# Performance work log

Hardware: AMD Instinct MI355X
Metric: run time of the kernel (lower is better)

The kernel has to match this reference:

```python
import jax, jax.numpy as jnp
import numpy as np

VOCAB = 128

def setup_inputs() -> dict:
    key = jax.random.key(0)
    k1, k2, k3, k4 = jax.random.split(key, 4)
    B, S, H = 64, 512, 1024
    x = jax.random.randint(k1, (B, S), 0, VOCAB, dtype=jnp.int32)
    h = jnp.zeros((B, H), dtype=jnp.float32)
    # Xavier-normal-ish scaled params
    W_xh = jax.random.normal(k2, (VOCAB, H), dtype=jnp.float32) * (2.0 / (VOCAB + H)) ** 0.5
    W_hh = jax.random.normal(k3, (H, H), dtype=jnp.float32) * (1.0 / H) ** 0.5
    b_h = jnp.zeros((H,), dtype=jnp.float32)
    W_out = jax.random.normal(k4, (H, VOCAB), dtype=jnp.float32) * (1.0 / H) ** 0.5
    b_out = jnp.zeros((VOCAB,), dtype=jnp.float32)
    return {"x": x, "h": h, "W_xh": W_xh, "W_hh": W_hh, "b_h": b_h,
            "W_out": W_out, "b_out": b_out}

def reference(x, h, W_xh, W_hh, b_h, W_out, b_out):
    """x: (B,S) int32, h: (B,H). Returns (logits (B,S,V), h_final (B,H)).
    one_hot(x) @ W_xh == embedding gather W_xh[x] (same math, no dense one-hot).
    Dropout is identity (eval mode). Sequential tanh recurrence via lax.scan."""
    x_emb = W_xh[x]                      # (B, S, H) gather == one-hot matmul
    x_emb_t = jnp.swapaxes(x_emb, 0, 1)  # (S, B, H) scan over time

    def step(h, xe):
        h_new = jnp.tanh(xe + h @ W_hh + b_h)
        return h_new, h_new

    h_final, hidden = jax.lax.scan(step, h, x_emb_t)  # hidden: (S, B, H)
    hidden = jnp.swapaxes(hidden, 0, 1)               # (B, S, H)
    logits = hidden @ W_out + b_out                   # (B, S, V)
    return logits, h_final
```

## Files before the change

kernel.cpp:

```cpp
#include <hip/hip_runtime.h>
#include <hip/hip_bf16.h>
#include <stdint.h>


#define Bz 64
#define Sz 512
#define Hz 1024
#define Vz 128
#define NWG 64
#define COLS 32
#define WGT 512

typedef __attribute__((ext_vector_type(8)))  short short8;
typedef __attribute__((ext_vector_type(16))) float f32x16;
typedef __attribute__((ext_vector_type(4)))  unsigned u32x4;

__device__ __align__(16) unsigned short g_hfrag[3][2][64][64][8];
__device__ __align__(16) unsigned short g_hidden[(size_t)Sz*2*64*64*8];
__device__ __align__(16) unsigned short g_wout[64*4*64*8];

__device__ __forceinline__ unsigned short f2bf(float f) {
  union { float f; unsigned u; } v; v.f = f;
  unsigned r = v.u + 0x7FFFu + ((v.u >> 16) & 1u);
  return (unsigned short)(r >> 16);
}

__device__ __forceinline__ float fast_tanh(float x) {
  float cx = fminf(9.0f, fmaxf(-9.0f, x));
  float e  = __builtin_amdgcn_exp2f(cx * 2.88539008178f);
  return (e - 1.0f) * __builtin_amdgcn_rcpf(e + 1.0f);
}

__device__ __forceinline__ void load8_nodrain(const unsigned short* p0, u32x4 t[8]) {
  const unsigned short* p1 = p0 + 2048;
  asm volatile(
    "global_load_dwordx4 %0, %8, off sc1\n\t"
    "global_load_dwordx4 %1, %8, off offset:1024 sc1\n\t"
    "global_load_dwordx4 %2, %8, off offset:2048 sc1\n\t"
    "global_load_dwordx4 %3, %8, off offset:3072 sc1\n\t"
    "global_load_dwordx4 %4, %9, off sc1\n\t"
    "global_load_dwordx4 %5, %9, off offset:1024 sc1\n\t"
    "global_load_dwordx4 %6, %9, off offset:2048 sc1\n\t"
    "global_load_dwordx4 %7, %9, off offset:3072 sc1"
    : "=&v"(t[0]), "=&v"(t[1]), "=&v"(t[2]), "=&v"(t[3]),
      "=&v"(t[4]), "=&v"(t[5]), "=&v"(t[6]), "=&v"(t[7])
    : "v"(p0), "v"(p1)
    : "memory");
}

__device__ __forceinline__ void store16_sc1(unsigned short* p, u32x4 v) {
  asm volatile("global_store_dwordx4 %0, %1, off sc1" :: "v"(p), "v"(v) : "memory");
}
__device__ __forceinline__ void store4_sc1(unsigned short* p, unsigned v) {
  asm volatile("global_store_dword %0, %1, off sc1" :: "v"(p), "v"(v) : "memory");
}

__global__ void pack_wout(const float* __restrict__ W_out) {
  int gid = blockIdx.x * blockDim.x + threadIdx.x;
  int lane = gid & 63;
  int nt   = (gid >> 6) & 3;
  int kb   = gid >> 8;
  int n = nt * 32 + (lane & 31);
  int k0 = kb * 16 + (lane >> 5) * 8;
  unsigned short t[8];
#pragma unroll
  for (int j = 0; j < 8; ++j)
    t[j] = f2bf(W_out[(size_t)(k0 + j) * Vz + n]);
  uint4 w;
  w.x = (unsigned)t[0] | ((unsigned)t[1] << 16);
  w.y = (unsigned)t[2] | ((unsigned)t[3] << 16);
  w.z = (unsigned)t[4] | ((unsigned)t[5] << 16);
  w.w = (unsigned)t[6] | ((unsigned)t[7] << 16);
  *(uint4*)&g_wout[(size_t)gid * 8] = w;
}

__global__ __launch_bounds__(WGT) void rnn_persistent(
    const int* __restrict__ x, const float* __restrict__ h0,
    const float* __restrict__ W_xh, const float* __restrict__ W_hh,
    const float* __restrict__ b_h, float* __restrict__ out,
    unsigned* __restrict__ flags)
{
  __shared__ unsigned short ldsW[64 * 64 * 8];
  __shared__ float red[8 * 1024];

  const int g    = blockIdx.x;
  const int bh   = g >> 5;
  const int cg   = g & 31;
  const int n0g  = cg * COLS;
  const int tid  = threadIdx.x;
  const int lane = tid & 63;
  const int ki   = tid >> 6;
  const int bn   = lane & 31;

  for (int idx = tid; idx < 64 * 64; idx += WGT) {
    int kb = idx >> 6, L = idx & 63;
    int n = L & 31, kq = L >> 5;
    unsigned short t[8];
#pragma unroll
    for (int j = 0; j < 8; ++j)
      t[j] = f2bf(W_hh[(size_t)(kb * 16 + kq * 8 + j) * Hz + n0g + n]);
    uint4 w;
    w.x = (unsigned)t[0] | ((unsigned)t[1] << 16);
    w.y = (unsigned)t[2] | ((unsigned)t[3] << 16);
    w.z = (unsigned)t[4] | ((unsigned)t[5] << 16);
    w.w = (unsigned)t[6] | ((unsigned)t[7] << 16);
    *(uint4*)&ldsW[(size_t)idx * 8] = w;
  }

  if (tid < 128) {
    int s_idx = g * 128 + tid;
    int fbh = s_idx >> 12, fkb = (s_idx >> 6) & 63, fL = s_idx & 63;
    int m = fbh * 32 + (fL & 31);
    int k = fkb * 16 + (fL >> 5) * 8;
    const float* src = &h0[(size_t)m * Hz + k];
    float4 a0 = *(const float4*)&src[0];
    float4 a1 = *(const float4*)&src[4];
    u32x4 w;
    w.x = (unsigned)f2bf(a0.x) | ((unsigned)f2bf(a0.y) << 16);
    w.y = (unsigned)f2bf(a0.z) | ((unsigned)f2bf(a0.w) << 16);
    w.z = (unsigned)f2bf(a1.x) | ((unsigned)f2bf(a1.y) << 16);
    w.w = (unsigned)f2bf(a1.z) | ((unsigned)f2bf(a1.w) << 16);
    store16_sc1(&g_hfrag[0][fbh][fkb][fL][0], w);
  }

  __syncthreads();
  asm volatile("s_waitcnt vmcnt(0)" ::: "memory");
  if (lane == 0)
    __hip_atomic_store(&flags[(g * 8 + ki) * 4], 1u, __ATOMIC_RELAXED,
                       __HIP_MEMORY_SCOPE_AGENT);

  const int er   = tid & 31;
  const int em   = bh * 32 + er;
  const int c0   = (tid >> 5) * 2;
  const int kcol = n0g + c0;
  const int kb_g = kcol >> 4;
  const int kq2  = (kcol >> 3) & 1;
  const int lslot = kq2 * 32 + er;
  const size_t slotOff =
      (((size_t)bh * 64 + kb_g) * 64 + lslot) * 8 + (kcol & 7);
  const float bias0 = b_h[kcol], bias1 = b_h[kcol + 1];

  const int pflag =
      ((bh * 32 + ki * 4 + (lane >> 3)) * 8 + (lane & 7)) * 4;

  int tok_n = x[em * Sz];
  float2 xv_n = *(const float2*)&W_xh[(size_t)tok_n * Hz + kcol];

  int rp = 0;
  for (int s = 0; s < Sz; ++s) {
    const int wp = (rp == 2) ? 0 : rp + 1;
    const unsigned tgt = (unsigned)(s + 1);

    {
      for (int it = 0; it < 65536; ++it) {
        unsigned v = 0xFFFFFFFFu;
        if (lane < 32)
          v = __hip_atomic_load(&flags[pflag], __ATOMIC_RELAXED,
                                __HIP_MEMORY_SCOPE_AGENT);
        if (__all(v >= tgt)) break;
        __builtin_amdgcn_s_sleep(1);
      }
      asm volatile("" ::: "memory");
    }

    u32x4 t[8];
    load8_nodrain(&g_hfrag[rp][bh][ki * 8][lane][0], t);
    f32x16 acc0 = {}, acc1 = {};

#define STAGE(J, CNT)                                                          \
    {                                                                          \
      asm volatile("s_waitcnt vmcnt(" #CNT ")"                                 \
                   : "+v"(t[2 * (J)]), "+v"(t[2 * (J) + 1]));                  \
      const int kbp = ki * 8 + 2 * (J);                                        \
      short8 ba = *(const short8*)&ldsW[(size_t)(kbp * 64 + lane) * 8];        \
      short8 bb = *(const short8*)&ldsW[(size_t)((kbp + 1) * 64 + lane) * 8];  \
      acc0 = __builtin_amdgcn_mfma_f32_32x32x16_bf16(*(short8*)&t[2 * (J)],    \
                                                     ba, acc0, 0, 0, 0);       \
      acc1 = __builtin_amdgcn_mfma_f32_32x32x16_bf16(*(short8*)&t[2 * (J) + 1],\
                                                     bb, acc1, 0, 0, 0);       \
    }
    STAGE(0, 6) STAGE(1, 4) STAGE(2, 2) STAGE(3, 0)
#undef STAGE

    float2 xv = xv_n;
    if (s + 1 < Sz) {
      int t2 = x[em * Sz + s + 1];
      xv_n = *(const float2*)&W_xh[(size_t)t2 * Hz + kcol];
    }

    __syncthreads();
    {
#pragma unroll
      for (int r = 0; r < 16; ++r) {
        int m = 4 * (lane >> 5) + (r & 3) + 8 * (r >> 2);
        red[ki * 1024 + m * 32 + (bn ^ m)] = acc0[r] + acc1[r];
      }
    }
    __syncthreads();

    float z0, z1;
    {
      const int o0 = er * 32 + (c0 ^ er);
      const int o1 = er * 32 + ((c0 + 1) ^ er);
      z0 = ((red[o0] + red[1024 + o0]) + (red[2048 + o0] + red[3072 + o0])) +
           ((red[4096 + o0] + red[5120 + o0]) + (red[6144 + o0] + red[7168 + o0]));
      z1 = ((red[o1] + red[1024 + o1]) + (red[2048 + o1] + red[3072 + o1])) +
           ((red[4096 + o1] + red[5120 + o1]) + (red[6144 + o1] + red[7168 + o1]));
    }
    z0 = fast_tanh(z0 + xv.x + bias0);
    z1 = fast_tanh(z1 + xv.y + bias1);

    unsigned w2 = (unsigned)f2bf(z0) | ((unsigned)f2bf(z1) << 16);

    store4_sc1(&((unsigned short*)g_hfrag)[(size_t)wp * 65536 + slotOff], w2);
    asm volatile("s_waitcnt vmcnt(0)" ::: "memory");
    if (lane == 0)
      __hip_atomic_store(&flags[(g * 8 + ki) * 4], (unsigned)(s + 2),
                         __ATOMIC_RELAXED, __HIP_MEMORY_SCOPE_AGENT);

    *(unsigned*)&g_hidden[(size_t)s * 65536 + slotOff] = w2;
    if (s == Sz - 1) {
      float* hf = out + (size_t)Bz * Sz * Vz + (size_t)em * Hz + kcol;
      hf[0] = z0; hf[1] = z1;
    }
    rp = wp;
  }
}

__global__ __launch_bounds__(256) void logits_gemm(
    const float* __restrict__ b_out, float* __restrict__ out)
{
  const int tid = threadIdx.x, lane = tid & 63, nt = tid >> 6;
  const int s = blockIdx.x >> 1, mi = blockIdx.x & 1;
  const unsigned short* ab = &g_hidden[((size_t)s * 8192 + (size_t)mi * 4096) * 8];

  f32x16 acc = {};
#pragma unroll 8
  for (int kb = 0; kb < 64; ++kb) {
    short8 a = *(const short8*)&ab[(size_t)(kb * 64 + lane) * 8];
    short8 b = *(const short8*)&g_wout[(size_t)((kb * 4 + nt) * 64 + lane) * 8];
    acc = __builtin_amdgcn_mfma_f32_32x32x16_bf16(a, b, acc, 0, 0, 0);
  }
  const int col = nt * 32 + (lane & 31);
  const float bo = b_out[col];
  const int rbase = 4 * (lane >> 5);
#pragma unroll
  for (int r = 0; r < 16; ++r) {
    int m = rbase + (r & 3) + 8 * (r >> 2);
    int em = mi * 32 + m;
    out[((size_t)em * Sz + s) * Vz + col] = acc[r] + bo;
  }
}

extern "C" void kernel_launch(void* const* d_in, const int* in_sizes, int n_in,
                              void* d_out, int out_size, void* d_ws, size_t ws_size,
                              hipStream_t stream) {
  const int*   x     = (const int*)d_in[0];
  const float* h0    = (const float*)d_in[1];
  const float* W_xh  = (const float*)d_in[2];
  const float* W_hh  = (const float*)d_in[3];
  const float* b_h   = (const float*)d_in[4];
  const float* W_out = (const float*)d_in[5];
  const float* b_out = (const float*)d_in[6];
  float* out = (float*)d_out;

  (void)hipMemsetAsync(d_ws, 0, 8192, stream);
  pack_wout<<<64, 256, 0, stream>>>(W_out);
  rnn_persistent<<<NWG, WGT, 0, stream>>>(x, h0, W_xh, W_hh, b_h, out,
                                          (unsigned*)d_ws);
  logits_gemm<<<Sz * 2, 256, 0, stream>>>(b_out, out);
}
```

Baseline: 1.592 ms.

## Replace flag-based step sync with per-word tagged hidden-state exchange

Removes the separate per-wave flag array and its store-drain-then-flag handshake. Each hidden-state word is now written together with an epoch- and step-tagged sequence word in a single 8-byte store, and consumers poll the data itself until every tag matches. This drops one round trip of latency per timestep (store wait plus flag publish plus flag poll before the load). In exchange the exchange buffer doubles in size, each poll loads 16 vectors instead of 8, and the memset is replaced by a global epoch counter bumped in pack_wout.

```diff
diff --git a/kernel.cpp b/kernel.cpp
--- a/kernel.cpp
+++ b/kernel.cpp
@@ -14,8 +14,11 @@
 typedef __attribute__((ext_vector_type(8)))  short short8;
 typedef __attribute__((ext_vector_type(16))) float f32x16;
 typedef __attribute__((ext_vector_type(4)))  unsigned u32x4;
-
-__device__ __align__(16) unsigned short g_hfrag[3][2][64][64][8];
+typedef __attribute__((ext_vector_type(2)))  unsigned u32x2;
+
+__device__ unsigned g_epoch;
+
+__device__ __align__(16) unsigned g_hx[3][2][64][64][8];
 __device__ __align__(16) unsigned short g_hidden[(size_t)Sz*2*64*64*8];
 __device__ __align__(16) unsigned short g_wout[64*4*64*8];
 
@@ -31,31 +34,42 @@
   return (e - 1.0f) * __builtin_amdgcn_rcpf(e + 1.0f);
 }
 
-__device__ __forceinline__ void load8_nodrain(const unsigned short* p0, u32x4 t[8]) {
-  const unsigned short* p1 = p0 + 2048;
+__device__ __forceinline__ void load16_seq(const unsigned* p0, u32x4 t[16]) {
+  const unsigned* p1 = p0 + 1024;
+  const unsigned* p2 = p0 + 2048;
+  const unsigned* p3 = p0 + 3072;
   asm volatile(
-    "global_load_dwordx4 %0, %8, off sc1\n\t"
-    "global_load_dwordx4 %1, %8, off offset:1024 sc1\n\t"
-    "global_load_dwordx4 %2, %8, off offset:2048 sc1\n\t"
-    "global_load_dwordx4 %3, %8, off offset:3072 sc1\n\t"
-    "global_load_dwordx4 %4, %9, off sc1\n\t"
-    "global_load_dwordx4 %5, %9, off offset:1024 sc1\n\t"
-    "global_load_dwordx4 %6, %9, off offset:2048 sc1\n\t"
-    "global_load_dwordx4 %7, %9, off offset:3072 sc1"
-    : "=&v"(t[0]), "=&v"(t[1]), "=&v"(t[2]), "=&v"(t[3]),
-      "=&v"(t[4]), "=&v"(t[5]), "=&v"(t[6]), "=&v"(t[7])
-    : "v"(p0), "v"(p1)
+    "global_load_dwordx4 %0,  %16, off sc1\n\t"
+    "global_load_dwordx4 %1,  %16, off offset:16 sc1\n\t"
+    "global_load_dwordx4 %2,  %16, off offset:2048 sc1\n\t"
+    "global_load_dwordx4 %3,  %16, off offset:2064 sc1\n\t"
+    "global_load_dwordx4 %4,  %17, off sc1\n\t"
+    "global_load_dwordx4 %5,  %17, off offset:16 sc1\n\t"
+    "global_load_dwordx4 %6,  %17, off offset:2048 sc1\n\t"
+    "global_load_dwordx4 %7,  %17, off offset:2064 sc1\n\t"
+    "global_load_dwordx4 %8,  %18, off sc1\n\t"
+    "global_load_dwordx4 %9,  %18, off offset:16 sc1\n\t"
+    "global_load_dwordx4 %10, %18, off offset:2048 sc1\n\t"
+    "global_load_dwordx4 %11, %18, off offset:2064 sc1\n\t"
+    "global_load_dwordx4 %12, %19, off sc1\n\t"
+    "global_load_dwordx4 %13, %19, off offset:16 sc1\n\t"
+    "global_load_dwordx4 %14, %19, off offset:2048 sc1\n\t"
+    "global_load_dwordx4 %15, %19, off offset:2064 sc1\n\t"
+    "s_waitcnt vmcnt(0)"
+    : "=&v"(t[0]), "=&v"(t[1]), "=&v"(t[2]),  "=&v"(t[3]),
+      "=&v"(t[4]), "=&v"(t[5]), "=&v"(t[6]),  "=&v"(t[7]),
+      "=&v"(t[8]), "=&v"(t[9]), "=&v"(t[10]), "=&v"(t[11]),
+      "=&v"(t[12]),"=&v"(t[13]),"=&v"(t[14]), "=&v"(t[15])
+    : "v"(p0), "v"(p1), "v"(p2), "v"(p3)
     : "memory");
 }
 
-__device__ __forceinline__ void store16_sc1(unsigned short* p, u32x4 v) {
-  asm volatile("global_store_dwordx4 %0, %1, off sc1" :: "v"(p), "v"(v) : "memory");
-}
-__device__ __forceinline__ void store4_sc1(unsigned short* p, unsigned v) {
-  asm volatile("global_store_dword %0, %1, off sc1" :: "v"(p), "v"(v) : "memory");
+__device__ __forceinline__ void store8_sc1(unsigned* p, u32x2 v) {
+  asm volatile("global_store_dwordx2 %0, %1, off sc1" :: "v"(p), "v"(v) : "memory");
 }
 
 __global__ void pack_wout(const float* __restrict__ W_out) {
+  if (blockIdx.x == 0 && threadIdx.x == 0) g_epoch = g_epoch + 1u;
   int gid = blockIdx.x * blockDim.x + threadIdx.x;
   int lane = gid & 63;
   int nt   = (gid >> 6) & 3;
@@ -77,8 +91,7 @@
 __global__ __launch_bounds__(WGT) void rnn_persistent(
     const int* __restrict__ x, const float* __restrict__ h0,
     const float* __restrict__ W_xh, const float* __restrict__ W_hh,
-    const float* __restrict__ b_h, float* __restrict__ out,
-    unsigned* __restrict__ flags)
+    const float* __restrict__ b_h, float* __restrict__ out)
 {
   __shared__ unsigned short ldsW[64 * 64 * 8];
   __shared__ float red[8 * 1024];
@@ -91,6 +104,7 @@
   const int lane = tid & 63;
   const int ki   = tid >> 6;
   const int bn   = lane & 31;
+  const unsigned epb = g_epoch << 10;
 
   for (int idx = tid; idx < 64 * 64; idx += WGT) {
     int kb = idx >> 6, L = idx & 63;
@@ -107,27 +121,21 @@
     *(uint4*)&ldsW[(size_t)idx * 8] = w;
   }
 
-  if (tid < 128) {
-    int s_idx = g * 128 + tid;
-    int fbh = s_idx >> 12, fkb = (s_idx >> 6) & 63, fL = s_idx & 63;
-    int m = fbh * 32 + (fL & 31);
-    int k = fkb * 16 + (fL >> 5) * 8;
+  {
+    int u  = g * 512 + tid;
+    int w  = u & 3;
+    int L  = (u >> 2) & 63;
+    int kb = (u >> 8) & 63;
+    int fb = (u >> 14) & 1;
+    int m  = fb * 32 + (L & 31);
+    int k  = kb * 16 + (L >> 5) * 8 + w * 2;
     const float* src = &h0[(size_t)m * Hz + k];
-    float4 a0 = *(const float4*)&src[0];
-    float4 a1 = *(const float4*)&src[4];
-    u32x4 w;
-    w.x = (unsigned)f2bf(a0.x) | ((unsigned)f2bf(a0.y) << 16);
-    w.y = (unsigned)f2bf(a0.z) | ((unsigned)f2bf(a0.w) << 16);
-    w.z = (unsigned)f2bf(a1.x) | ((unsigned)f2bf(a1.y) << 16);
-    w.w = (unsigned)f2bf(a1.z) | ((unsigned)f2bf(a1.w) << 16);
-    store16_sc1(&g_hfrag[0][fbh][fkb][fL][0], w);
-  }
-
+    u32x2 v;
+    v.x = (unsigned)f2bf(src[0]) | ((unsigned)f2bf(src[1]) << 16);
+    v.y = epb + 1u;
+    store8_sc1(&g_hx[0][fb][kb][L][2 * w], v);
+  }
   __syncthreads();
-  asm volatile("s_waitcnt vmcnt(0)" ::: "memory");
-  if (lane == 0)
-    __hip_atomic_store(&flags[(g * 8 + ki) * 4], 1u, __ATOMIC_RELAXED,
-                       __HIP_MEMORY_SCOPE_AGENT);
 
   const int er   = tid & 31;
   const int em   = bh * 32 + er;
@@ -136,12 +144,11 @@
   const int kb_g = kcol >> 4;
   const int kq2  = (kcol >> 3) & 1;
   const int lslot = kq2 * 32 + er;
-  const size_t slotOff =
-      (((size_t)bh * 64 + kb_g) * 64 + lslot) * 8 + (kcol & 7);
+  const int wq   = (c0 >> 1) & 3;
+  unsigned* exw0 = &g_hx[0][bh][kb_g][lslot][2 * wq];
+  const size_t hidOff =
+      ((((size_t)bh * 64) + kb_g) * 64 + lslot) * 8 + (kcol & 7);
   const float bias0 = b_h[kcol], bias1 = b_h[kcol + 1];
-
-  const int pflag =
-      ((bh * 32 + ki * 4 + (lane >> 3)) * 8 + (lane & 7)) * 4;
 
   int tok_n = x[em * Sz];
   float2 xv_n = *(const float2*)&W_xh[(size_t)tok_n * Hz + kcol];
@@ -149,38 +156,40 @@
   int rp = 0;
   for (int s = 0; s < Sz; ++s) {
     const int wp = (rp == 2) ? 0 : rp + 1;
-    const unsigned tgt = (unsigned)(s + 1);
-
+    const unsigned tgt = epb + (unsigned)(s + 1);
+
+    u32x4 t[16];
     {
-      for (int it = 0; it < 65536; ++it) {
-        unsigned v = 0xFFFFFFFFu;
-        if (lane < 32)
-          v = __hip_atomic_load(&flags[pflag], __ATOMIC_RELAXED,
-                                __HIP_MEMORY_SCOPE_AGENT);
-        if (__all(v >= tgt)) break;
+      const unsigned* hp = &g_hx[rp][bh][ki * 8][lane][0];
+      const int bound = (s == 0) ? 65536 : 8192;
+      for (int it = 0; it < bound; ++it) {
+        load16_seq(hp, t);
+        unsigned bad = (t[0].y ^ tgt) | (t[0].w ^ tgt);
+#pragma unroll
+        for (int i = 1; i < 16; ++i)
+          bad |= (t[i].y ^ tgt) | (t[i].w ^ tgt);
+        if (__all(bad == 0u)) break;
         __builtin_amdgcn_s_sleep(1);
       }
       asm volatile("" ::: "memory");
     }
 
-    u32x4 t[8];
-    load8_nodrain(&g_hfrag[rp][bh][ki * 8][lane][0], t);
     f32x16 acc0 = {}, acc1 = {};
-
-#define STAGE(J, CNT)                                                          \
-    {                                                                          \
-      asm volatile("s_waitcnt vmcnt(" #CNT ")"                                 \
-                   : "+v"(t[2 * (J)]), "+v"(t[2 * (J) + 1]));                  \
-      const int kbp = ki * 8 + 2 * (J);                                        \
-      short8 ba = *(const short8*)&ldsW[(size_t)(kbp * 64 + lane) * 8];        \
-      short8 bb = *(const short8*)&ldsW[(size_t)((kbp + 1) * 64 + lane) * 8];  \
-      acc0 = __builtin_amdgcn_mfma_f32_32x32x16_bf16(*(short8*)&t[2 * (J)],    \
-                                                     ba, acc0, 0, 0, 0);       \
-      acc1 = __builtin_amdgcn_mfma_f32_32x32x16_bf16(*(short8*)&t[2 * (J) + 1],\
-                                                     bb, acc1, 0, 0, 0);       \
-    }
-    STAGE(0, 6) STAGE(1, 4) STAGE(2, 2) STAGE(3, 0)
-#undef STAGE
+#pragma unroll
+    for (int p = 0; p < 8; p += 2) {
+      u32x4 fa, fb2;
+      fa.x  = t[2 * p].x;     fa.y  = t[2 * p].z;
+      fa.z  = t[2 * p + 1].x; fa.w  = t[2 * p + 1].z;
+      fb2.x = t[2 * p + 2].x; fb2.y = t[2 * p + 2].z;
+      fb2.z = t[2 * p + 3].x; fb2.w = t[2 * p + 3].z;
+      const int kbp = ki * 8 + p;
+      short8 ba = *(const short8*)&ldsW[(size_t)(kbp * 64 + lane) * 8];
+      short8 bb = *(const short8*)&ldsW[(size_t)((kbp + 1) * 64 + lane) * 8];
+      acc0 = __builtin_amdgcn_mfma_f32_32x32x16_bf16(*(short8*)&fa, ba,
+                                                     acc0, 0, 0, 0);
+      acc1 = __builtin_amdgcn_mfma_f32_32x32x16_bf16(*(short8*)&fb2, bb,
+                                                     acc1, 0, 0, 0);
+    }
 
     float2 xv = xv_n;
     if (s + 1 < Sz) {
@@ -212,13 +221,10 @@
 
     unsigned w2 = (unsigned)f2bf(z0) | ((unsigned)f2bf(z1) << 16);
 
-    store4_sc1(&((unsigned short*)g_hfrag)[(size_t)wp * 65536 + slotOff], w2);
-    asm volatile("s_waitcnt vmcnt(0)" ::: "memory");
-    if (lane == 0)
-      __hip_atomic_store(&flags[(g * 8 + ki) * 4], (unsigned)(s + 2),
-                         __ATOMIC_RELAXED, __HIP_MEMORY_SCOPE_AGENT);
-
-    *(unsigned*)&g_hidden[(size_t)s * 65536 + slotOff] = w2;
+    u32x2 v; v.x = w2; v.y = epb + (unsigned)(s + 2);
+    store8_sc1(exw0 + (size_t)wp * 65536, v);
+
+    *(unsigned*)&g_hidden[(size_t)s * 65536 + hidOff] = w2;
     if (s == Sz - 1) {
       float* hf = out + (size_t)Bz * Sz * Vz + (size_t)em * Hz + kcol;
       hf[0] = z0; hf[1] = z1;
@@ -264,9 +270,7 @@
   const float* b_out = (const float*)d_in[6];
   float* out = (float*)d_out;
 
-  (void)hipMemsetAsync(d_ws, 0, 8192, stream);
   pack_wout<<<64, 256, 0, stream>>>(W_out);
-  rnn_persistent<<<NWG, WGT, 0, stream>>>(x, h0, W_xh, W_hh, b_h, out,
-                                          (unsigned*)d_ws);
+  rnn_persistent<<<NWG, WGT, 0, stream>>>(x, h0, W_xh, W_hh, b_h, out);
   logits_gemm<<<Sz * 2, 256, 0, stream>>>(b_out, out);
 }
```

After: 1.980 ms. +24.4%, slower.

## Use 16 workgroups with register-resident W_hh and LDS-staged hidden state

Applied to the files above, without the earlier changes.

Cuts the persistent RNN grid from 64 to 16 workgroups, each owning 64 output columns across the full batch. The W_hh slice is kept in registers as bf16 MFMA fragments instead of LDS, and the full hidden state is staged into LDS every step. Synchronisation changes from per-wave fine-grained flags to a single flag per workgroup, polled by one wave after a block barrier. The aim is to shrink per-step cross-workgroup sync cost, at the price of fewer CUs doing the matmul, more hidden-state traffic per workgroup, heavy register pressure, and extra barriers per step.

```diff
diff --git a/kernel.cpp b/kernel.cpp
--- a/kernel.cpp
+++ b/kernel.cpp
@@ -7,15 +7,16 @@
 #define Sz 512
 #define Hz 1024
 #define Vz 128
-#define NWG 64
-#define COLS 32
+#define NWG 16
+#define COLS 64
 #define WGT 512
 
 typedef __attribute__((ext_vector_type(8)))  short short8;
 typedef __attribute__((ext_vector_type(16))) float f32x16;
+typedef __attribute__((ext_vector_type(4)))  float f32x4;
 typedef __attribute__((ext_vector_type(4)))  unsigned u32x4;
 
-__device__ __align__(16) unsigned short g_hfrag[3][2][64][64][8];
+__device__ __align__(16) unsigned short g_hx2[3][2][64][64][8];
 __device__ __align__(16) unsigned short g_hidden[(size_t)Sz*2*64*64*8];
 __device__ __align__(16) unsigned short g_wout[64*4*64*8];
 
@@ -31,28 +32,37 @@
   return (e - 1.0f) * __builtin_amdgcn_rcpf(e + 1.0f);
 }
 
-__device__ __forceinline__ void load8_nodrain(const unsigned short* p0, u32x4 t[8]) {
+__device__ __forceinline__ void load16_nodrain(const unsigned short* p0, u32x4 t[16]) {
   const unsigned short* p1 = p0 + 2048;
+  const unsigned short* p2 = p0 + 4096;
+  const unsigned short* p3 = p0 + 6144;
   asm volatile(
-    "global_load_dwordx4 %0, %8, off sc1\n\t"
-    "global_load_dwordx4 %1, %8, off offset:1024 sc1\n\t"
-    "global_load_dwordx4 %2, %8, off offset:2048 sc1\n\t"
-    "global_load_dwordx4 %3, %8, off offset:3072 sc1\n\t"
-    "global_load_dwordx4 %4, %9, off sc1\n\t"
-    "global_load_dwordx4 %5, %9, off offset:1024 sc1\n\t"
-    "global_load_dwordx4 %6, %9, off offset:2048 sc1\n\t"
-    "global_load_dwordx4 %7, %9, off offset:3072 sc1"
-    : "=&v"(t[0]), "=&v"(t[1]), "=&v"(t[2]), "=&v"(t[3]),
-      "=&v"(t[4]), "=&v"(t[5]), "=&v"(t[6]), "=&v"(t[7])
-    : "v"(p0), "v"(p1)
+    "global_load_dwordx4 %0,  %16, off sc1\n\t"
+    "global_load_dwordx4 %1,  %16, off offset:1024 sc1\n\t"
+    "global_load_dwordx4 %2,  %16, off offset:2048 sc1\n\t"
+    "global_load_dwordx4 %3,  %16, off offset:3072 sc1\n\t"
+    "global_load_dwordx4 %4,  %17, off sc1\n\t"
+    "global_load_dwordx4 %5,  %17, off offset:1024 sc1\n\t"
+    "global_load_dwordx4 %6,  %17, off offset:2048 sc1\n\t"
+    "global_load_dwordx4 %7,  %17, off offset:3072 sc1\n\t"
+    "global_load_dwordx4 %8,  %18, off sc1\n\t"
+    "global_load_dwordx4 %9,  %18, off offset:1024 sc1\n\t"
+    "global_load_dwordx4 %10, %18, off offset:2048 sc1\n\t"
+    "global_load_dwordx4 %11, %18, off offset:3072 sc1\n\t"
+    "global_load_dwordx4 %12, %19, off sc1\n\t"
+    "global_load_dwordx4 %13, %19, off offset:1024 sc1\n\t"
+    "global_load_dwordx4 %14, %19, off offset:2048 sc1\n\t"
+    "global_load_dwordx4 %15, %19, off offset:3072 sc1"
+    : "=&v"(t[0]), "=&v"(t[1]), "=&v"(t[2]),  "=&v"(t[3]),
+      "=&v"(t[4]), "=&v"(t[5]), "=&v"(t[6]),  "=&v"(t[7]),
+      "=&v"(t[8]), "=&v"(t[9]), "=&v"(t[10]), "=&v"(t[11]),
+      "=&v"(t[12]),"=&v"(t[13]),"=&v"(t[14]), "=&v"(t[15])
+    : "v"(p0), "v"(p1), "v"(p2), "v"(p3)
     : "memory");
 }
 
 __device__ __forceinline__ void store16_sc1(unsigned short* p, u32x4 v) {
   asm volatile("global_store_dwordx4 %0, %1, off sc1" :: "v"(p), "v"(v) : "memory");
-}
-__device__ __forceinline__ void store4_sc1(unsigned short* p, unsigned v) {
-  asm volatile("global_store_dword %0, %1, off sc1" :: "v"(p), "v"(v) : "memory");
 }
 
 __global__ void pack_wout(const float* __restrict__ W_out) {
@@ -74,45 +84,48 @@
   *(uint4*)&g_wout[(size_t)gid * 8] = w;
 }
 
-__global__ __launch_bounds__(WGT) void rnn_persistent(
+__global__ __launch_bounds__(WGT, 2) void rnn_persistent(
     const int* __restrict__ x, const float* __restrict__ h0,
     const float* __restrict__ W_xh, const float* __restrict__ W_hh,
     const float* __restrict__ b_h, float* __restrict__ out,
     unsigned* __restrict__ flags)
 {
-  __shared__ unsigned short ldsW[64 * 64 * 8];
-  __shared__ float red[8 * 1024];
+  __shared__ unsigned short hstage[2 * 64 * 64 * 8];
+  __shared__ float red[4 * 1024];
 
   const int g    = blockIdx.x;
-  const int bh   = g >> 5;
-  const int cg   = g & 31;
-  const int n0g  = cg * COLS;
+  const int n0g  = g * COLS;
   const int tid  = threadIdx.x;
   const int lane = tid & 63;
   const int ki   = tid >> 6;
-  const int bn   = lane & 31;
-
-  for (int idx = tid; idx < 64 * 64; idx += WGT) {
-    int kb = idx >> 6, L = idx & 63;
-    int n = L & 31, kq = L >> 5;
-    unsigned short t[8];
-#pragma unroll
-    for (int j = 0; j < 8; ++j)
-      t[j] = f2bf(W_hh[(size_t)(kb * 16 + kq * 8 + j) * Hz + n0g + n]);
-    uint4 w;
-    w.x = (unsigned)t[0] | ((unsigned)t[1] << 16);
-    w.y = (unsigned)t[2] | ((unsigned)t[3] << 16);
-    w.z = (unsigned)t[4] | ((unsigned)t[5] << 16);
-    w.w = (unsigned)t[6] | ((unsigned)t[7] << 16);
-    *(uint4*)&ldsW[(size_t)idx * 8] = w;
-  }
-
-  if (tid < 128) {
-    int s_idx = g * 128 + tid;
-    int fbh = s_idx >> 12, fkb = (s_idx >> 6) & 63, fL = s_idx & 63;
-    int m = fbh * 32 + (fL & 31);
-    int k = fkb * 16 + (fL >> 5) * 8;
-    const float* src = &h0[(size_t)m * Hz + k];
+  const int mt   = ki >> 2;
+  const int nt   = (ki >> 1) & 1;
+  const int kt   = ki & 1;
+
+  short8 wfrag[32];
+  {
+    const int col = n0g + nt * 32 + (lane & 31);
+    const float* wbase = &W_hh[(size_t)(kt * 512 + (lane >> 5) * 8) * Hz + col];
+#pragma unroll
+    for (int ks = 0; ks < 32; ++ks) {
+      const float* wp_ = wbase + (size_t)ks * 16 * Hz;
+      unsigned short tt[8];
+#pragma unroll
+      for (int j = 0; j < 8; ++j) tt[j] = f2bf(wp_[(size_t)j * Hz]);
+      short8 w;
+      w[0] = (short)tt[0]; w[1] = (short)tt[1]; w[2] = (short)tt[2]; w[3] = (short)tt[3];
+      w[4] = (short)tt[4]; w[5] = (short)tt[5]; w[6] = (short)tt[6]; w[7] = (short)tt[7];
+      wfrag[ks] = w;
+    }
+  }
+
+  {
+    int u = g * 512 + tid;
+    int slot = u & 63, plane = u >> 6;
+    int kb = plane & 63, fmt = plane >> 6;
+    int m  = fmt * 32 + (slot & 31);
+    int k0 = kb * 16 + (slot >> 5) * 8;
+    const float* src = &h0[(size_t)m * Hz + k0];
     float4 a0 = *(const float4*)&src[0];
     float4 a1 = *(const float4*)&src[4];
     u32x4 w;
@@ -120,31 +133,36 @@
     w.y = (unsigned)f2bf(a0.z) | ((unsigned)f2bf(a0.w) << 16);
     w.z = (unsigned)f2bf(a1.x) | ((unsigned)f2bf(a1.y) << 16);
     w.w = (unsigned)f2bf(a1.z) | ((unsigned)f2bf(a1.w) << 16);
-    store16_sc1(&g_hfrag[0][fbh][fkb][fL][0], w);
-  }
-
+    store16_sc1(&((unsigned short*)g_hx2)[(size_t)u * 8], w);
+  }
   __syncthreads();
-  asm volatile("s_waitcnt vmcnt(0)" ::: "memory");
-  if (lane == 0)
-    __hip_atomic_store(&flags[(g * 8 + ki) * 4], 1u, __ATOMIC_RELAXED,
+  if (tid == 0)
+    __hip_atomic_store(&flags[g * 8], 1u, __ATOMIC_RELAXED,
                        __HIP_MEMORY_SCOPE_AGENT);
 
-  const int er   = tid & 31;
-  const int em   = bh * 32 + er;
-  const int c0   = (tid >> 5) * 2;
-  const int kcol = n0g + c0;
-  const int kb_g = kcol >> 4;
-  const int kq2  = (kcol >> 3) & 1;
-  const int lslot = kq2 * 32 + er;
-  const size_t slotOff =
-      (((size_t)bh * 64 + kb_g) * 64 + lslot) * 8 + (kcol & 7);
-  const float bias0 = b_h[kcol], bias1 = b_h[kcol + 1];
-
-  const int pflag =
-      ((bh * 32 + ki * 4 + (lane >> 3)) * 8 + (lane & 7)) * 4;
-
-  int tok_n = x[em * Sz];
-  float2 xv_n = *(const float2*)&W_xh[(size_t)tok_n * Hz + kcol];
+  const int er  = tid & 63;
+  const int jo  = tid >> 6;
+  const int rr  = er & 31, emt = er >> 5, ent = jo >> 2;
+  const int reg = (rr & 3) + 4 * (rr >> 3);
+  const int lh  = (rr >> 2) & 1;
+  const int redbase = (emt * 2 + ent) * 1024 + (reg >> 2) * 256 +
+                      ((jo & 3) * 8 + 32 * lh) * 4 + (reg & 3);
+  const int kbE   = g * 4 + (jo >> 1);
+  const int slotE = (jo & 1) * 32 + rr;
+  const size_t exOff  = (((size_t)emt * 64 + kbE) * 64 + slotE) * 8;
+  const size_t hidOff = exOff;
+  float bias[8];
+#pragma unroll
+  for (int j = 0; j < 8; ++j) bias[j] = b_h[n0g + jo * 8 + j];
+
+  int tok_n = x[er * Sz];
+  float4 xa_n = *(const float4*)&W_xh[(size_t)tok_n * Hz + n0g + jo * 8];
+  float4 xb_n = *(const float4*)&W_xh[(size_t)tok_n * Hz + n0g + jo * 8 + 4];
+
+  const int stbase = ki * 1024;
+  const short8* hs8 = (const short8*)hstage;
+  u32x4* hsv = (u32x4*)hstage;
+  const int abase = (mt * 64 + kt * 32) * 64;
 
   int rp = 0;
   for (int s = 0; s < Sz; ++s) {
@@ -152,77 +170,105 @@
     const unsigned tgt = (unsigned)(s + 1);
 
     {
-      for (int it = 0; it < 65536; ++it) {
+      const int bound = (s == 0) ? 131072 : 16384;
+      for (int it = 0; it < bound; ++it) {
         unsigned v = 0xFFFFFFFFu;
-        if (lane < 32)
-          v = __hip_atomic_load(&flags[pflag], __ATOMIC_RELAXED,
+        if (lane < NWG)
+          v = __hip_atomic_load(&flags[lane * 8], __ATOMIC_RELAXED,
                                 __HIP_MEMORY_SCOPE_AGENT);
         if (__all(v >= tgt)) break;
         __builtin_amdgcn_s_sleep(1);
       }
       asm volatile("" ::: "memory");
     }
-
-    u32x4 t[8];
-    load8_nodrain(&g_hfrag[rp][bh][ki * 8][lane][0], t);
+    __syncthreads();
+
+    u32x4 t[16];
+    load16_nodrain(((const unsigned short*)g_hx2) + (size_t)rp * 65536 +
+                       ki * 8192 + lane * 8, t);
+#define STG(J, CNT)                                                            \
+    { asm volatile("s_waitcnt vmcnt(" #CNT ")"                                 \
+                   : "+v"(t[4*(J)]), "+v"(t[4*(J)+1]),                         \
+                     "+v"(t[4*(J)+2]), "+v"(t[4*(J)+3]));                      \
+      hsv[stbase + (4*(J)+0) * 64 + lane] = t[4*(J)+0];                        \
+      hsv[stbase + (4*(J)+1) * 64 + lane] = t[4*(J)+1];                        \
+      hsv[stbase + (4*(J)+2) * 64 + lane] = t[4*(J)+2];                        \
+      hsv[stbase + (4*(J)+3) * 64 + lane] = t[4*(J)+3]; }
+    STG(0, 12) STG(1, 8) STG(2, 4) STG(3, 0)
+#undef STG
+    __syncthreads();
+
     f32x16 acc0 = {}, acc1 = {};
-
-#define STAGE(J, CNT)                                                          \
-    {                                                                          \
-      asm volatile("s_waitcnt vmcnt(" #CNT ")"                                 \
-                   : "+v"(t[2 * (J)]), "+v"(t[2 * (J) + 1]));                  \
-      const int kbp = ki * 8 + 2 * (J);                                        \
-      short8 ba = *(const short8*)&ldsW[(size_t)(kbp * 64 + lane) * 8];        \
-      short8 bb = *(const short8*)&ldsW[(size_t)((kbp + 1) * 64 + lane) * 8];  \
-      acc0 = __builtin_amdgcn_mfma_f32_32x32x16_bf16(*(short8*)&t[2 * (J)],    \
-                                                     ba, acc0, 0, 0, 0);       \
-      acc1 = __builtin_amdgcn_mfma_f32_32x32x16_bf16(*(short8*)&t[2 * (J) + 1],\
-                                                     bb, acc1, 0, 0, 0);       \
-    }
-    STAGE(0, 6) STAGE(1, 4) STAGE(2, 2) STAGE(3, 0)
-#undef STAGE
-
-    float2 xv = xv_n;
+#pragma unroll
+    for (int ks = 0; ks < 32; ks += 2) {
+      short8 a0 = hs8[abase + (ks + 0) * 64 + lane];
+      short8 a1 = hs8[abase + (ks + 1) * 64 + lane];
+      acc0 = __builtin_amdgcn_mfma_f32_32x32x16_bf16(a0, wfrag[ks],     acc0, 0, 0, 0);
+      acc1 = __builtin_amdgcn_mfma_f32_32x32x16_bf16(a1, wfrag[ks + 1], acc1, 0, 0, 0);
+    }
+#pragma unroll
+    for (int r = 0; r < 16; ++r) acc0[r] += acc1[r];
+
+    float4 xa = xa_n, xb = xb_n;
     if (s + 1 < Sz) {
-      int t2 = x[em * Sz + s + 1];
-      xv_n = *(const float2*)&W_xh[(size_t)t2 * Hz + kcol];
-    }
-
-    __syncthreads();
-    {
-#pragma unroll
-      for (int r = 0; r < 16; ++r) {
-        int m = 4 * (lane >> 5) + (r & 3) + 8 * (r >> 2);
-        red[ki * 1024 + m * 32 + (bn ^ m)] = acc0[r] + acc1[r];
+      int t2 = x[er * Sz + s + 1];
+      xa_n = *(const float4*)&W_xh[(size_t)t2 * Hz + n0g + jo * 8];
+      xb_n = *(const float4*)&W_xh[(size_t)t2 * Hz + n0g + jo * 8 + 4];
+    }
+
+    if (kt == 1) {
+      const int rb = (mt * 2 + nt) * 1024;
+#pragma unroll
+      for (int r2 = 0; r2 < 4; ++r2) {
+        f32x4 w = {acc0[4*r2], acc0[4*r2+1], acc0[4*r2+2], acc0[4*r2+3]};
+        *(f32x4*)&red[rb + r2 * 256 + lane * 4] = w;
       }
     }
     __syncthreads();
-
-    float z0, z1;
-    {
-      const int o0 = er * 32 + (c0 ^ er);
-      const int o1 = er * 32 + ((c0 + 1) ^ er);
-      z0 = ((red[o0] + red[1024 + o0]) + (red[2048 + o0] + red[3072 + o0])) +
-           ((red[4096 + o0] + red[5120 + o0]) + (red[6144 + o0] + red[7168 + o0]));
-      z1 = ((red[o1] + red[1024 + o1]) + (red[2048 + o1] + red[3072 + o1])) +
-           ((red[4096 + o1] + red[5120 + o1]) + (red[6144 + o1] + red[7168 + o1]));
-    }
-    z0 = fast_tanh(z0 + xv.x + bias0);
-    z1 = fast_tanh(z1 + xv.y + bias1);
-
-    unsigned w2 = (unsigned)f2bf(z0) | ((unsigned)f2bf(z1) << 16);
-
-    store4_sc1(&((unsigned short*)g_hfrag)[(size_t)wp * 65536 + slotOff], w2);
-    asm volatile("s_waitcnt vmcnt(0)" ::: "memory");
-    if (lane == 0)
-      __hip_atomic_store(&flags[(g * 8 + ki) * 4], (unsigned)(s + 2),
-                         __ATOMIC_RELAXED, __HIP_MEMORY_SCOPE_AGENT);
-
-    *(unsigned*)&g_hidden[(size_t)s * 65536 + slotOff] = w2;
+    if (kt == 0) {
+      const int rb = (mt * 2 + nt) * 1024;
+#pragma unroll
+      for (int r2 = 0; r2 < 4; ++r2) {
+        f32x4 p = *(const f32x4*)&red[rb + r2 * 256 + lane * 4];
+        f32x4 w = {acc0[4*r2] + p.x, acc0[4*r2+1] + p.y,
+                   acc0[4*r2+2] + p.z, acc0[4*r2+3] + p.w};
+        *(f32x4*)&red[rb + r2 * 256 + lane * 4] = w;
+      }
+    }
+    __syncthreads();
+
+    float z[8];
+#pragma unroll
+    for (int i = 0; i < 8; ++i) z[i] = red[redbase + i * 4];
+    z[0] = fast_tanh(z[0] + xa.x + bias[0]);
+    z[1] = fast_tanh(z[1] + xa.y + bias[1]);
+    z[2] = fast_tanh(z[2] + xa.z + bias[2]);
+    z[3] = fast_tanh(z[3] + xa.w + bias[3]);
+    z[4] = fast_tanh(z[4] + xb.x + bias[4]);
+    z[5] = fast_tanh(z[5] + xb.y + bias[5]);
+    z[6] = fast_tanh(z[6] + xb.z + bias[6]);
+    z[7] = fast_tanh(z[7] + xb.w + bias[7]);
+
+    u32x4 w2;
+    w2.x = (unsigned)f2bf(z[0]) | ((unsigned)f2bf(z[1]) << 16);
+    w2.y = (unsigned)f2bf(z[2]) | ((unsigned)f2bf(z[3]) << 16);
+    w2.z = (unsigned)f2bf(z[4]) | ((unsigned)f2bf(z[5]) << 16);
+    w2.w = (unsigned)f2bf(z[6]) | ((unsigned)f2bf(z[7]) << 16);
+
+    store16_sc1(&((unsigned short*)g_hx2)[(size_t)wp * 65536 + exOff], w2);
+    *(u32x4*)&g_hidden[(size_t)s * 65536 + hidOff] = w2;
     if (s == Sz - 1) {
-      float* hf = out + (size_t)Bz * Sz * Vz + (size_t)em * Hz + kcol;
-      hf[0] = z0; hf[1] = z1;
-    }
+      float* hf = out + (size_t)Bz * Sz * Vz + (size_t)er * Hz + n0g + jo * 8;
+      float4 f0 = {z[0], z[1], z[2], z[3]};
+      float4 f1 = {z[4], z[5], z[6], z[7]};
+      *(float4*)&hf[0] = f0;
+      *(float4*)&hf[4] = f1;
+    }
+
+    __syncthreads();
+    if (tid == 0)
+      __hip_atomic_store(&flags[g * 8], (unsigned)(s + 2), __ATOMIC_RELAXED,
+                         __HIP_MEMORY_SCOPE_AGENT);
     rp = wp;
   }
 }
@@ -264,7 +310,7 @@
   const float* b_out = (const float*)d_in[6];
   float* out = (float*)d_out;
 
-  (void)hipMemsetAsync(d_ws, 0, 8192, stream);
+  (void)hipMemsetAsync(d_ws, 0, 4096, stream);
   pack_wout<<<64, 256, 0, stream>>>(W_out);
   rnn_persistent<<<NWG, WGT, 0, stream>>>(x, h0, W_xh, W_hh, b_h, out,
                                           (unsigned*)d_ws);
```

Result: slower. 2.486 ms (+56.2%).

## Halve persistent workgroups and interleave two batch halves per workgroup

Applied to the files above, without the earlier changes.

The persistent RNN kernel now runs 32 workgroups instead of 64. Each workgroup owns a 32-column slice for both batch halves and alternates their time steps inside one loop. The aim is to hide the cross-workgroup flag wait and the global-memory latency of one batch half behind the compute of the other, and to cut the number of agents taking part in each barrier. In exchange each workgroup does twice the serial work per step, and with half the CUs busy the per-step critical path may grow.

```diff
diff --git a/kernel.cpp b/kernel.cpp
--- a/kernel.cpp
+++ b/kernel.cpp
@@ -7,7 +7,7 @@
 #define Sz 512
 #define Hz 1024
 #define Vz 128
-#define NWG 64
+#define NWG 32
 #define COLS 32
 #define WGT 512
 
@@ -84,9 +84,7 @@
   __shared__ float red[8 * 1024];
 
   const int g    = blockIdx.x;
-  const int bh   = g >> 5;
-  const int cg   = g & 31;
-  const int n0g  = cg * COLS;
+  const int n0g  = g * COLS;
   const int tid  = threadIdx.x;
   const int lane = tid & 63;
   const int ki   = tid >> 6;
@@ -107,8 +105,8 @@
     *(uint4*)&ldsW[(size_t)idx * 8] = w;
   }
 
-  if (tid < 128) {
-    int s_idx = g * 128 + tid;
+  if (tid < 256) {
+    int s_idx = g * 256 + tid;
     int fbh = s_idx >> 12, fkb = (s_idx >> 6) & 63, fL = s_idx & 63;
     int m = fbh * 32 + (fL & 31);
     int k = fkb * 16 + (fL >> 5) * 8;
@@ -125,33 +123,32 @@
 
   __syncthreads();
   asm volatile("s_waitcnt vmcnt(0)" ::: "memory");
-  if (lane == 0)
-    __hip_atomic_store(&flags[(g * 8 + ki) * 4], 1u, __ATOMIC_RELAXED,
-                       __HIP_MEMORY_SCOPE_AGENT);
+  if (lane == 0) {
+    __hip_atomic_store(&flags[((0 * 32 + g) * 8 + ki) * 4], 1u,
+                       __ATOMIC_RELAXED, __HIP_MEMORY_SCOPE_AGENT);
+    __hip_atomic_store(&flags[((1 * 32 + g) * 8 + ki) * 4], 1u,
+                       __ATOMIC_RELAXED, __HIP_MEMORY_SCOPE_AGENT);
+  }
 
   const int er   = tid & 31;
-  const int em   = bh * 32 + er;
   const int c0   = (tid >> 5) * 2;
   const int kcol = n0g + c0;
   const int kb_g = kcol >> 4;
   const int kq2  = (kcol >> 3) & 1;
   const int lslot = kq2 * 32 + er;
-  const size_t slotOff =
-      (((size_t)bh * 64 + kb_g) * 64 + lslot) * 8 + (kcol & 7);
   const float bias0 = b_h[kcol], bias1 = b_h[kcol + 1];
 
-  const int pflag =
-      ((bh * 32 + ki * 4 + (lane >> 3)) * 8 + (lane & 7)) * 4;
-
-  int tok_n = x[em * Sz];
-  float2 xv_n = *(const float2*)&W_xh[(size_t)tok_n * Hz + kcol];
-
-  int rp = 0;
-  for (int s = 0; s < Sz; ++s) {
-    const int wp = (rp == 2) ? 0 : rp + 1;
+  const int emA = 0 * 32 + er, emB = 1 * 32 + er;
+  float2 xvA_n = *(const float2*)&W_xh[(size_t)x[emA * Sz] * Hz + kcol];
+  float2 xvB_n = *(const float2*)&W_xh[(size_t)x[emB * Sz] * Hz + kcol];
+
+  auto stream_step = [&](int sbh, float2& xvn, int s, int rp, int wp) {
     const unsigned tgt = (unsigned)(s + 1);
+    const int em = sbh * 32 + er;
 
     {
+      const int pflag =
+          ((sbh * 32 + ki * 4 + (lane >> 3)) * 8 + (lane & 7)) * 4;
       for (int it = 0; it < 65536; ++it) {
         unsigned v = 0xFFFFFFFFu;
         if (lane < 32)
@@ -164,7 +161,7 @@
     }
 
     u32x4 t[8];
-    load8_nodrain(&g_hfrag[rp][bh][ki * 8][lane][0], t);
+    load8_nodrain(&g_hfrag[rp][sbh][ki * 8][lane][0], t);
     f32x16 acc0 = {}, acc1 = {};
 
 #define STAGE(J, CNT)                                                          \
@@ -182,10 +179,10 @@
     STAGE(0, 6) STAGE(1, 4) STAGE(2, 2) STAGE(3, 0)
 #undef STAGE
 
-    float2 xv = xv_n;
+    float2 xv = xvn;
     if (s + 1 < Sz) {
       int t2 = x[em * Sz + s + 1];
-      xv_n = *(const float2*)&W_xh[(size_t)t2 * Hz + kcol];
+      xvn = *(const float2*)&W_xh[(size_t)t2 * Hz + kcol];
     }
 
     __syncthreads();
@@ -212,17 +209,27 @@
 
     unsigned w2 = (unsigned)f2bf(z0) | ((unsigned)f2bf(z1) << 16);
 
+    const size_t slotOff =
+        (((size_t)sbh * 64 + kb_g) * 64 + lslot) * 8 + (kcol & 7);
     store4_sc1(&((unsigned short*)g_hfrag)[(size_t)wp * 65536 + slotOff], w2);
     asm volatile("s_waitcnt vmcnt(0)" ::: "memory");
     if (lane == 0)
-      __hip_atomic_store(&flags[(g * 8 + ki) * 4], (unsigned)(s + 2),
-                         __ATOMIC_RELAXED, __HIP_MEMORY_SCOPE_AGENT);
+      __hip_atomic_store(&flags[((sbh * 32 + g) * 8 + ki) * 4],
+                         (unsigned)(s + 2), __ATOMIC_RELAXED,
+                         __HIP_MEMORY_SCOPE_AGENT);
 
     *(unsigned*)&g_hidden[(size_t)s * 65536 + slotOff] = w2;
     if (s == Sz - 1) {
       float* hf = out + (size_t)Bz * Sz * Vz + (size_t)em * Hz + kcol;
       hf[0] = z0; hf[1] = z1;
     }
+  };
+
+  int rp = 0;
+  for (int s = 0; s < Sz; ++s) {
+    const int wp = (rp == 2) ? 0 : rp + 1;
+    stream_step(0, xvA_n, s, rp, wp);
+    stream_step(1, xvB_n, s, rp, wp);
     rp = wp;
   }
 }
```

New measurement: 2.816 ms. 1.77x slower.
